# Kernel tuning notes

Measured on AMD Instinct MI355X. Metric: run time of the kernel, lower is better.

Reference implementation:

```python
import jax, jax.numpy as jnp
import numpy as np

TEMP = 2.0   # NTXent uses a hardcoded temperature of 2, not the ctor's 0.07
EPS = 1e-8   # F.cosine_similarity eps


def setup_inputs() -> dict:
    key = jax.random.key(0)
    k1, _ = jax.random.split(key)
    x = jax.random.normal(k1, (8192, 256), dtype=jnp.float32)
    unused = jnp.zeros((1,), dtype=jnp.int32)
    return {"x": x, "unused": unused}


def _cos_matrix(a, b):
    # pairwise cosine similarity: [N, N]
    na = jnp.linalg.norm(a, axis=-1)
    nb = jnp.linalg.norm(b, axis=-1)
    dots = a @ b.T
    return dots / jnp.maximum(na[:, None] * nb[None, :], EPS)


def reference(x, unused):
    n = x.shape[0] // 2
    p, q = x[:n], x[n:]  # anchor, positive

    s_pp = _cos_matrix(p, p)
    s_pn = _cos_matrix(p, q)
    s_nn = _cos_matrix(q, q)
    s_np = _cos_matrix(q, p)

    # double loop i, j in [i, n): upper triangle including diagonal
    mask = jnp.triu(jnp.ones((n, n), dtype=bool))

    exp_sum = (jnp.exp(s_pp / TEMP) + jnp.exp(s_pn / TEMP)
               + jnp.exp(s_nn / TEMP) + jnp.exp(s_np / TEMP))
    sim_all = jnp.sum(jnp.where(mask, exp_sum, 0.0))

    sim_s = jnp.sum(jnp.exp(jnp.diagonal(s_pn) / TEMP))

    return -jnp.log(sim_s / sim_all)
```

## Files before the change

### kernel.cpp

```cpp
#include <hip/hip_runtime.h>

#define DIM     256
#define NROWS   8192
#define NTILE   64
#define NBLK    ((NTILE * (NTILE + 1)) / 2)
#define GB      520
#define TPB     4
#define NPART   (GB * 4)
#define CHPLANE ((size_t)NROWS * 16)

using i32x4  = __attribute__((ext_vector_type(4))) int;
using i32x8  = __attribute__((ext_vector_type(8))) int;
using f32x16 = __attribute__((ext_vector_type(16))) float;

struct i32x8_pair { i32x4 lo, hi; };

__device__ __forceinline__ unsigned fp4q(float v) {
  float a = fabsf(v);
  unsigned s = (__builtin_bit_cast(unsigned, v) >> 31) << 3;
  unsigned c = a < 0.25f ? 0u : a < 0.75f ? 1u : a < 1.25f ? 2u : a < 1.75f ? 3u
             : a < 2.50f ? 4u : a < 3.50f ? 5u : a < 7u;
  c = a < 0.25f ? 0u : a < 0.75f ? 1u : a < 1.25f ? 2u : a < 1.75f ? 3u
    : a < 2.50f ? 4u : a < 3.50f ? 5u : a < 5.00f ? 6u : 7u;
  return s | c;
}

__device__ __forceinline__ void tile_rc(int t, int& bi, int& bj) {
  int i = (int)((129.0 - sqrt(129.0 * 129.0 - 8.0 * (double)t)) * 0.5);
  while ((i * (129 - i)) / 2 > t) --i;
  while (((i + 1) * (128 - i)) / 2 <= t) ++i;
  bi = i;
  bj = i + (t - (i * (129 - i)) / 2);
}

__device__ __forceinline__ float exp_half(float x) {
  float t = x * 0.7213475204444817f;
  float r;
  asm("v_exp_f32 %0, %1" : "=v"(r) : "v"(t));
  return r;
}

__global__ __launch_bounds__(256) void normalize_k(const float* __restrict__ x,
                                                   unsigned char* __restrict__ z4) {
  const int row  = blockIdx.x * 4 + (threadIdx.x >> 6);
  const int lane = threadIdx.x & 63;
  float4 v = ((const float4*)(x + (size_t)row * DIM))[lane];
  float ss = v.x * v.x + v.y * v.y + v.z * v.z + v.w * v.w;
#pragma unroll
  for (int off = 32; off > 0; off >>= 1) ss += __shfl_xor(ss, off, 64);
  float rn = rsqrtf(fmaxf(ss, 1e-24f)) * 16.0f;
  unsigned c0 = fp4q(v.x * rn), c1 = fp4q(v.y * rn);
  unsigned c2 = fp4q(v.z * rn), c3 = fp4q(v.w * rn);
  unsigned short pk = (unsigned short)((c0 | (c1 << 4)) | ((c2 | (c3 << 4)) << 8));
  *(unsigned short*)(z4 + (size_t)(lane >> 3) * CHPLANE
                        + (size_t)row * 16 + ((2 * lane) & 14)) = pk;
}

__global__ __launch_bounds__(256, 2) void gram_k(const unsigned char* __restrict__ z4,
                                                 double2* __restrict__ partial) {
  const int tid   = threadIdx.x;
  const int lane  = tid & 63;
  const int w     = tid >> 6;
  const int wr    = w >> 1, wc = w & 1;
  const int l31   = lane & 31;
  const int khalf = lane >> 5;

  double accS = 0.0, accD = 0.0;
  const i32x4 zero4 = {0, 0, 0, 0};

#pragma unroll 1
  for (int k = 0; k < TPB; ++k) {
    int bi, bj; tile_rc(blockIdx.x + k * GB, bi, bj);

    const unsigned char* baseA = z4 + (size_t)khalf * CHPLANE
                               + ((size_t)bi * 128 + wr * 64 + l31) * 16;
    const unsigned char* baseB = z4 + (size_t)khalf * CHPLANE
                               + ((size_t)bj * 128 + wc * 64 + l31) * 16;

    i32x4 af[4][2], bf[4][2];
#pragma unroll
    for (int kc = 0; kc < 4; ++kc)
#pragma unroll
      for (int t = 0; t < 2; ++t) {
        af[kc][t] = *(const i32x4*)(baseA + (size_t)(2 * kc) * CHPLANE + t * 512);
        bf[kc][t] = *(const i32x4*)(baseB + (size_t)(2 * kc) * CHPLANE + t * 512);
      }

    f32x16 acc_f[2][2] = {};
#pragma unroll
    for (int kc = 0; kc < 4; ++kc) {
#pragma unroll
      for (int ti = 0; ti < 2; ++ti)
#pragma unroll
        for (int tj = 0; tj < 2; ++tj) {
          i32x8_pair pa = { af[kc][ti], zero4 };
          i32x8_pair pb = { bf[kc][tj], zero4 };
          acc_f[ti][tj] = __builtin_amdgcn_mfma_scale_f32_32x32x64_f8f6f4(
              __builtin_bit_cast(i32x8, pa), __builtin_bit_cast(i32x8, pb),
              acc_f[ti][tj],
              4, 4,
              0, 0x7B7B7B7B,
              0, 0x7B7B7B7B);
        }
    }

    const bool tdiag = (bi == bj);
    const bool sdiag = (bj == bi + 32);
    float ls[4] = {0.f, 0.f, 0.f, 0.f};
    float dsum = 0.0f;
    if (tdiag || sdiag) {
#pragma unroll
      for (int ti = 0; ti < 2; ++ti)
#pragma unroll
        for (int tj = 0; tj < 2; ++tj)
#pragma unroll
          for (int r = 0; r < 16; ++r) {
            float e = exp_half(acc_f[ti][tj][r]);
            ls[r & 3] += e;
            int row_l = (r & 3) + 8 * (r >> 2) + 4 * khalf;
            if (wr == wc && ti == tj && row_l == l31) dsum += e;
          }
    } else {
#pragma unroll
      for (int ti = 0; ti < 2; ++ti)
#pragma unroll
        for (int tj = 0; tj < 2; ++tj)
#pragma unroll
          for (int r = 0; r < 16; ++r)
            ls[r & 3] += exp_half(acc_f[ti][tj][r]);
    }
    float lsum = (ls[0] + ls[1]) + (ls[2] + ls[3]);
    accS += tdiag ? (double)lsum + (double)dsum : 2.0 * (double)lsum;
    if (sdiag) accD += (double)dsum;
  }

#pragma unroll
  for (int off = 32; off > 0; off >>= 1) {
    accS += __shfl_xor(accS, off, 64);
    accD += __shfl_xor(accD, off, 64);
  }
  if (lane == 0) {
    double2 v; v.x = accS; v.y = accD;
    partial[blockIdx.x * 4 + w] = v;
  }
}

__global__ __launch_bounds__(256) void reduce_k(const double2* __restrict__ partial,
                                               float* __restrict__ out) {
  __shared__ double redS[4], redD[4];
  double s = 0.0, ss = 0.0;
  for (int i = threadIdx.x; i < NPART; i += 256) {
    double2 v = partial[i];
    s += v.x; ss += v.y;
  }
#pragma unroll
  for (int off = 32; off > 0; off >>= 1) {
    s  += __shfl_xor(s,  off, 64);
    ss += __shfl_xor(ss, off, 64);
  }
  const int w = threadIdx.x >> 6;
  if ((threadIdx.x & 63) == 0) { redS[w] = s; redD[w] = ss; }
  __syncthreads();
  if (threadIdx.x == 0) {
    double S  = (redS[0] + redS[1]) + (redS[2] + redS[3]);
    double sd = (redD[0] + redD[1]) + (redD[2] + redD[3]);
    out[0] = (float)(log(0.5 * S + sd) - log(sd));
  }
}

extern "C" void kernel_launch(void* const* d_in, const int* in_sizes, int n_in,
                              void* d_out, int out_size, void* d_ws, size_t ws_size,
                              hipStream_t stream) {
  const float* x    = (const float*)d_in[0];
  unsigned char* z4 = (unsigned char*)d_ws;
  double2* partial  = (double2*)((char*)d_ws + 8 * CHPLANE);
  float* out        = (float*)d_out;

  normalize_k<<<dim3(NROWS / 4), dim3(256), 0, stream>>>(x, z4);
  gram_k<<<dim3(GB), dim3(256), 0, stream>>>(z4, partial);
  reduce_k<<<dim3(1), dim3(256), 0, stream>>>(partial, out);
}
```

Baseline: 75.54 us.

## Split each gram tile across two blocks, one tile per block, higher occupancy

Removes the four-tiles-per-block loop. Each 128x128 triangular tile is now split between two blocks by row half, and each wave computes a 64x32 sub-block. The grid grows from 520 to 4160 blocks and launch bounds allow 4 blocks per CU, which aims to balance load and hide memory latency across more waves. In exchange each wave reuses its loaded operands less, and the reduce kernel has many more partials to sum. The malformed duplicate quantization expression is also cleaned up.

Result: slower. 89.54 us (+18.5%).

```diff
diff --git a/kernel.cpp b/kernel.cpp
--- a/kernel.cpp
+++ b/kernel.cpp
@@ -4,8 +4,7 @@
 #define NROWS   8192
 #define NTILE   64
 #define NBLK    ((NTILE * (NTILE + 1)) / 2)
-#define GB      520
-#define TPB     4
+#define GB      (NBLK * 2)
 #define NPART   (GB * 4)
 #define CHPLANE ((size_t)NROWS * 16)
 
@@ -19,9 +18,7 @@
   float a = fabsf(v);
   unsigned s = (__builtin_bit_cast(unsigned, v) >> 31) << 3;
   unsigned c = a < 0.25f ? 0u : a < 0.75f ? 1u : a < 1.25f ? 2u : a < 1.75f ? 3u
-             : a < 2.50f ? 4u : a < 3.50f ? 5u : a < 7u;
-  c = a < 0.25f ? 0u : a < 0.75f ? 1u : a < 1.25f ? 2u : a < 1.75f ? 3u
-    : a < 2.50f ? 4u : a < 3.50f ? 5u : a < 5.00f ? 6u : 7u;
+             : a < 2.50f ? 4u : a < 3.50f ? 5u : a < 5.00f ? 6u : 7u;
   return s | c;
 }
 
@@ -56,91 +53,79 @@
                         + (size_t)row * 16 + ((2 * lane) & 14)) = pk;
 }
 
-__global__ __launch_bounds__(256, 2) void gram_k(const unsigned char* __restrict__ z4,
+__global__ __launch_bounds__(256, 4) void gram_k(const unsigned char* __restrict__ z4,
                                                  double2* __restrict__ partial) {
   const int tid   = threadIdx.x;
   const int lane  = tid & 63;
   const int w     = tid >> 6;
-  const int wr    = w >> 1, wc = w & 1;
   const int l31   = lane & 31;
   const int khalf = lane >> 5;
 
-  double accS = 0.0, accD = 0.0;
+  const int h = blockIdx.x & 1;
+  int bi, bj; tile_rc(blockIdx.x >> 1, bi, bj);
+
+  const unsigned char* baseA = z4 + (size_t)khalf * CHPLANE
+                             + ((size_t)bi * 128 + h * 64 + l31) * 16;
+  const unsigned char* baseB = z4 + (size_t)khalf * CHPLANE
+                             + ((size_t)bj * 128 + w * 32 + l31) * 16;
+
+  i32x4 af[2][4], bf[4];
+#pragma unroll
+  for (int kc = 0; kc < 4; ++kc) {
+    af[0][kc] = *(const i32x4*)(baseA + (size_t)(2 * kc) * CHPLANE);
+    af[1][kc] = *(const i32x4*)(baseA + (size_t)(2 * kc) * CHPLANE + 512);
+    bf[kc]    = *(const i32x4*)(baseB + (size_t)(2 * kc) * CHPLANE);
+  }
+
+  f32x16 acc[2] = {};
   const i32x4 zero4 = {0, 0, 0, 0};
+#pragma unroll
+  for (int kc = 0; kc < 4; ++kc) {
+#pragma unroll
+    for (int rt = 0; rt < 2; ++rt) {
+      i32x8_pair pa = { af[rt][kc], zero4 };
+      i32x8_pair pb = { bf[kc],     zero4 };
+      acc[rt] = __builtin_amdgcn_mfma_scale_f32_32x32x64_f8f6f4(
+          __builtin_bit_cast(i32x8, pa), __builtin_bit_cast(i32x8, pb),
+          acc[rt],
+          4, 4,
+          0, 0x7B7B7B7B,
+          0, 0x7B7B7B7B);
+    }
+  }
 
-#pragma unroll 1
-  for (int k = 0; k < TPB; ++k) {
-    int bi, bj; tile_rc(blockIdx.x + k * GB, bi, bj);
-
-    const unsigned char* baseA = z4 + (size_t)khalf * CHPLANE
-                               + ((size_t)bi * 128 + wr * 64 + l31) * 16;
-    const unsigned char* baseB = z4 + (size_t)khalf * CHPLANE
-                               + ((size_t)bj * 128 + wc * 64 + l31) * 16;
-
-    i32x4 af[4][2], bf[4][2];
+  const bool tdiag = (bi == bj);
+  const bool sdiag = (bj == bi + 32);
+  float ls[4] = {0.f, 0.f, 0.f, 0.f};
+  float dsum = 0.0f;
+  if (tdiag || sdiag) {
 #pragma unroll
-    for (int kc = 0; kc < 4; ++kc)
+    for (int rt = 0; rt < 2; ++rt)
 #pragma unroll
-      for (int t = 0; t < 2; ++t) {
-        af[kc][t] = *(const i32x4*)(baseA + (size_t)(2 * kc) * CHPLANE + t * 512);
-        bf[kc][t] = *(const i32x4*)(baseB + (size_t)(2 * kc) * CHPLANE + t * 512);
+      for (int r = 0; r < 16; ++r) {
+        float e = exp_half(acc[rt][r]);
+        ls[r & 3] += e;
+        int row_l = (r & 3) + 8 * (r >> 2) + 4 * khalf;
+        if (w == 2 * h + rt && row_l == l31) dsum += e;
       }
-
-    f32x16 acc_f[2][2] = {};
+  } else {
 #pragma unroll
-    for (int kc = 0; kc < 4; ++kc) {
+    for (int rt = 0; rt < 2; ++rt)
 #pragma unroll
-      for (int ti = 0; ti < 2; ++ti)
-#pragma unroll
-        for (int tj = 0; tj < 2; ++tj) {
-          i32x8_pair pa = { af[kc][ti], zero4 };
-          i32x8_pair pb = { bf[kc][tj], zero4 };
-          acc_f[ti][tj] = __builtin_amdgcn_mfma_scale_f32_32x32x64_f8f6f4(
-              __builtin_bit_cast(i32x8, pa), __builtin_bit_cast(i32x8, pb),
-              acc_f[ti][tj],
-              4, 4,
-              0, 0x7B7B7B7B,
-              0, 0x7B7B7B7B);
-        }
-    }
-
-    const bool tdiag = (bi == bj);
-    const bool sdiag = (bj == bi + 32);
-    float ls[4] = {0.f, 0.f, 0.f, 0.f};
-    float dsum = 0.0f;
-    if (tdiag || sdiag) {
-#pragma unroll
-      for (int ti = 0; ti < 2; ++ti)
-#pragma unroll
-        for (int tj = 0; tj < 2; ++tj)
-#pragma unroll
-          for (int r = 0; r < 16; ++r) {
-            float e = exp_half(acc_f[ti][tj][r]);
-            ls[r & 3] += e;
-            int row_l = (r & 3) + 8 * (r >> 2) + 4 * khalf;
-            if (wr == wc && ti == tj && row_l == l31) dsum += e;
-          }
-    } else {
-#pragma unroll
-      for (int ti = 0; ti < 2; ++ti)
-#pragma unroll
-        for (int tj = 0; tj < 2; ++tj)
-#pragma unroll
-          for (int r = 0; r < 16; ++r)
-            ls[r & 3] += exp_half(acc_f[ti][tj][r]);
-    }
-    float lsum = (ls[0] + ls[1]) + (ls[2] + ls[3]);
-    accS += tdiag ? (double)lsum + (double)dsum : 2.0 * (double)lsum;
-    if (sdiag) accD += (double)dsum;
+      for (int r = 0; r < 16; ++r)
+        ls[r & 3] += exp_half(acc[rt][r]);
   }
+  float lsum = (ls[0] + ls[1]) + (ls[2] + ls[3]);
+  double aS = tdiag ? (double)lsum + (double)dsum : 2.0 * (double)lsum;
+  double aD = sdiag ? (double)dsum : 0.0;
 
 #pragma unroll
   for (int off = 32; off > 0; off >>= 1) {
-    accS += __shfl_xor(accS, off, 64);
-    accD += __shfl_xor(accD, off, 64);
+    aS += __shfl_xor(aS, off, 64);
+    aD += __shfl_xor(aD, off, 64);
   }
   if (lane == 0) {
-    double2 v; v.x = accS; v.y = accD;
+    double2 v; v.x = aS; v.y = aD;
     partial[blockIdx.x * 4 + w] = v;
   }
 }
```
